# Performance work log

Measured on AMD Instinct MI355X. Metric: run time of the kernel, lower is better.

The kernel has to match this reference:

```python
import jax, jax.numpy as jnp
import numpy as np

H = 4096          # hidden_size
NQ = 32           # num query heads
NKV = 8           # num kv heads
D = 128           # head_dim
GRP = NQ // NKV   # query heads per kv head
THETA = 10000.0
SCALE = D ** -0.5


def _rope(x, positions):
    # x: [S, N, D]; neox-style rotate-half over full head_dim
    half = D // 2
    inv_freq = 1.0 / (THETA ** (jnp.arange(0, half, dtype=jnp.float32) / half * 2.0 * 0.5 * 2))
    inv_freq = 1.0 / (THETA ** (jnp.arange(0, D, 2, dtype=jnp.float32) / D))
    freqs = positions.astype(jnp.float32)[:, None] * inv_freq[None, :]  # [S, D/2]
    cos = jnp.cos(freqs)[:, None, :]  # [S,1,D/2]
    sin = jnp.sin(freqs)[:, None, :]
    x1, x2 = x[..., :half], x[..., half:]
    return jnp.concatenate([x1 * cos - x2 * sin, x2 * cos + x1 * sin], axis=-1)


def setup_inputs() -> dict:
    key = jax.random.key(0)
    k1, k2, k3 = jax.random.split(key, 3)
    S = 4096
    return {
        "positions": jnp.arange(S, dtype=jnp.int64 if jax.config.jax_enable_x64 else jnp.int32),
        "hidden_states": jax.random.normal(k1, (S, H), dtype=jnp.float32) * 0.02,
        "w_qkv": jax.random.normal(k2, (H, NQ * D + 2 * NKV * D), dtype=jnp.float32) * 0.02,
        "w_o": jax.random.normal(k3, (NQ * D, H), dtype=jnp.float32) * 0.02,
    }


def reference(positions, hidden_states, w_qkv, w_o):
    S = hidden_states.shape[0]
    qkv = hidden_states @ w_qkv                         # [S, 6144]
    q, k, v = jnp.split(qkv, [NQ * D, NQ * D + NKV * D], axis=-1)
    q = _rope(q.reshape(S, NQ, D), positions)           # [S, NQ, D]
    k = _rope(k.reshape(S, NKV, D), positions)          # [S, NKV, D]
    v = v.reshape(S, NKV, D)
    # GQA: group query heads per kv head
    qg = q.reshape(S, NKV, GRP, D)
    scores = jnp.einsum('sghd,tgd->ghst', qg, k) * SCALE  # [NKV, GRP, S, S]
    causal = positions[:, None] >= positions[None, :]     # [S, S]
    scores = jnp.where(causal[None, None], scores, jnp.finfo(scores.dtype).min)
    probs = jax.nn.softmax(scores, axis=-1)
    attn = jnp.einsum('ghst,tgd->sghd', probs, v).reshape(S, NQ * D)
    return attn @ w_o
```

## Files before the change

kernel.cpp:

```cpp
#include <hip/hip_runtime.h>
#include <hip/hip_bf16.h>
#include <math.h>

#define H_DIM 4096
#define NQ    32
#define NKV   8
#define HD    128
#define GRPQ  4
#define NQKV  6144
#define KOFF  4096
#define VOFF  5120
#define SCALE 0.08838834764831844f

typedef float f32x4 __attribute__((ext_vector_type(4)));
typedef short bf16x8 __attribute__((ext_vector_type(8)));

static __device__ __forceinline__ float bf2f(unsigned short u) {
    return __uint_as_float(((unsigned int)u) << 16);
}
static __device__ __forceinline__ unsigned short f2bf(float f) {
    return __bfloat16_as_ushort(__float2bfloat16(f));
}

static __device__ __forceinline__ void gload_lds16(const void* g, void* l) {
    __builtin_amdgcn_global_load_lds(
        (const __attribute__((address_space(1))) unsigned int*)g,
        (__attribute__((address_space(3))) unsigned int*)l, 16, 0, 0);
}

static __device__ __forceinline__ float4 load4(const float* p) {
    return *reinterpret_cast<const float4*>(p);
}
static __device__ __forceinline__ float4 load4(const unsigned short* p) {
    ushort4 v = *reinterpret_cast<const ushort4*>(p);
    return make_float4(bf2f(v.x), bf2f(v.y), bf2f(v.z), bf2f(v.w));
}

static __device__ __forceinline__ void store1(float* p, float v) { *p = v; }
static __device__ __forceinline__ void store1(unsigned short* p, float v) {
    *p = f2bf(v);
}

#define BM 128
#define BN 128
#define BK 16
#define LPAD 4

template <typename TA, typename TB, typename TC>
__global__ __launch_bounds__(256) void gemm_f32acc(
    const TA* __restrict__ A,
    const TB* __restrict__ B,
    TC* __restrict__ C,
    int M, int N, int K)
{
    __shared__ float As[BK][BM + LPAD];
    __shared__ float Bs[BK][BN + LPAD];

    const int tid = threadIdx.x;
    const int bm  = blockIdx.y * BM;
    const int bn  = blockIdx.x * BN;
    const int tx  = tid & 15;
    const int ty  = tid >> 4;

    float acc[8][8];
#pragma unroll
    for (int i = 0; i < 8; ++i)
#pragma unroll
        for (int j = 0; j < 8; ++j) acc[i][j] = 0.0f;

    for (int k0 = 0; k0 < K; k0 += BK) {
        for (int q = tid; q < (BM * BK) / 4; q += 256) {
            int row = q >> 2;
            int kq  = (q & 3) << 2;
            float4 v = load4(&A[(size_t)(bm + row) * K + k0 + kq]);
            As[kq + 0][row] = v.x;
            As[kq + 1][row] = v.y;
            As[kq + 2][row] = v.z;
            As[kq + 3][row] = v.w;
        }
        for (int q = tid; q < (BK * BN) / 4; q += 256) {
            int k = q >> 5;
            int n = (q & 31) << 2;
            float4 v = load4(&B[(size_t)(k0 + k) * N + bn + n]);
            Bs[k][n + 0] = v.x;
            Bs[k][n + 1] = v.y;
            Bs[k][n + 2] = v.z;
            Bs[k][n + 3] = v.w;
        }
        __syncthreads();

#pragma unroll
        for (int k = 0; k < BK; ++k) {
            float a[8], b[8];
#pragma unroll
            for (int i = 0; i < 8; ++i) a[i] = As[k][ty * 8 + i];
#pragma unroll
            for (int j = 0; j < 8; ++j) b[j] = Bs[k][tx * 8 + j];
#pragma unroll
            for (int i = 0; i < 8; ++i)
#pragma unroll
                for (int j = 0; j < 8; ++j) acc[i][j] += a[i] * b[j];
        }
        __syncthreads();
    }

#pragma unroll
    for (int i = 0; i < 8; ++i) {
        size_t r = (size_t)(bm + ty * 8 + i);
#pragma unroll
        for (int j = 0; j < 8; ++j) {
            int c = bn + tx * 8 + j;
            store1(&C[r * N + c], acc[i][j]);
        }
    }
}

__global__ __launch_bounds__(256) void cvt_f32_bf16(
    const float4* __restrict__ src, ushort4* __restrict__ dst, int n4)
{
    int i = blockIdx.x * 256 + threadIdx.x;
    int stride = gridDim.x * 256;
    for (; i < n4; i += stride) {
        float4 v = src[i];
        dst[i] = make_ushort4(f2bf(v.x), f2bf(v.y), f2bf(v.z), f2bf(v.w));
    }
}

__global__ __launch_bounds__(256) void transpose_f32_bf16(
    const float* __restrict__ src, unsigned short* __restrict__ dst,
    int R, int C)
{
    __shared__ unsigned short tile[32][33];
    const int r0 = blockIdx.y * 32;
    const int c0 = blockIdx.x * 32;
    const int t  = threadIdx.x;
    const int lr  = t >> 3;
    const int lc4 = (t & 7) << 2;

    float4 v = load4(&src[(size_t)(r0 + lr) * C + c0 + lc4]);
    tile[lr][lc4 + 0] = f2bf(v.x);
    tile[lr][lc4 + 1] = f2bf(v.y);
    tile[lr][lc4 + 2] = f2bf(v.z);
    tile[lr][lc4 + 3] = f2bf(v.w);
    __syncthreads();

    ushort4 o = make_ushort4(tile[lc4 + 0][lr], tile[lc4 + 1][lr],
                             tile[lc4 + 2][lr], tile[lc4 + 3][lr]);
    *reinterpret_cast<ushort4*>(&dst[(size_t)(c0 + lr) * R + r0 + lc4]) = o;
}

template <typename TC>
__global__ __launch_bounds__(256) void gemm_bf16_bt(
    const unsigned short* __restrict__ A,
    const unsigned short* __restrict__ BT,
    TC* __restrict__ C,
    int M, int N, int K)
{
    __shared__ unsigned short As[128 * 32];
    __shared__ unsigned short Bs[128 * 32];

    const int tid  = threadIdx.x;
    const int lane = tid & 63;
    const int w    = tid >> 6;
    const int wr   = w >> 1;
    const int wc   = w & 1;
    const int l15  = lane & 15;
    const int l4   = lane >> 4;
    const size_t bm = (size_t)blockIdx.y * 128;
    const size_t bn = (size_t)blockIdx.x * 128;

    f32x4 acc[4][4];
#pragma unroll
    for (int mi = 0; mi < 4; ++mi)
#pragma unroll
        for (int ni = 0; ni < 4; ++ni) acc[mi][ni] = (f32x4){0.f, 0.f, 0.f, 0.f};

    for (int k0 = 0; k0 < K; k0 += 32) {
        __syncthreads();
#pragma unroll
        for (int it = 0; it < 2; ++it) {
            const int cb = (w * 2 + it) * 64;
            const int c  = cb + lane;
            gload_lds16(A  + (bm + (c >> 2)) * K + k0 + (c & 3) * 8,
                        (char*)As + cb * 16);
            gload_lds16(BT + (bn + (c >> 2)) * K + k0 + (c & 3) * 8,
                        (char*)Bs + cb * 16);
        }
        __syncthreads();

        bf16x8 a[4], b[4];
#pragma unroll
        for (int mi = 0; mi < 4; ++mi)
            a[mi] = *reinterpret_cast<const bf16x8*>(
                (char*)As + (wr * 64 + mi * 16 + l15) * 64 + l4 * 16);
#pragma unroll
        for (int ni = 0; ni < 4; ++ni)
            b[ni] = *reinterpret_cast<const bf16x8*>(
                (char*)Bs + (wc * 64 + ni * 16 + l15) * 64 + l4 * 16);
#pragma unroll
        for (int mi = 0; mi < 4; ++mi)
#pragma unroll
            for (int ni = 0; ni < 4; ++ni)
                acc[mi][ni] = __builtin_amdgcn_mfma_f32_16x16x32_bf16(
                    a[mi], b[ni], acc[mi][ni], 0, 0, 0);
    }

#pragma unroll
    for (int mi = 0; mi < 4; ++mi) {
#pragma unroll
        for (int r = 0; r < 4; ++r) {
            size_t row = bm + wr * 64 + mi * 16 + l4 * 4 + r;
#pragma unroll
            for (int ni = 0; ni < 4; ++ni) {
                size_t col = bn + wc * 64 + ni * 16 + l15;
                store1(&C[row * N + col], acc[mi][ni][r]);
            }
        }
    }
}

__global__ __launch_bounds__(256) void rope_kernel(
    unsigned short* __restrict__ qkv,
    const int* __restrict__ pos32,
    int S)
{
    int idx = blockIdx.x * 256 + threadIdx.x;
    int total = S * (NQ + NKV) * (HD / 2);
    if (idx >= total) return;

    int j    = idx & 63;
    int head = (idx >> 6) % (NQ + NKV);
    int s    = idx / (64 * (NQ + NKV));

    const bool is64 = (pos32[1] == 0);
    int pos = is64 ? pos32[2 * s] : pos32[s];

    unsigned short* row = qkv + (size_t)s * NQKV + head * HD;
    float x1 = bf2f(row[j]);
    float x2 = bf2f(row[j + 64]);

    float p = (float)pos;
    float inv_freq = powf(10000.0f, -((float)j) * (1.0f / 64.0f));
    float f = p * inv_freq;
    float sn, cs;
    sincosf(f, &sn, &cs);

    row[j]      = f2bf(x1 * cs - x2 * sn);
    row[j + 64] = f2bf(x2 * cs + x1 * sn);
}

__global__ __launch_bounds__(256) void attn_mfma(
    const unsigned short* __restrict__ qkv,
    unsigned short* __restrict__ attn_out,
    int S)
{
    __shared__ unsigned short Ks[64 * 128];
    __shared__ unsigned short Vts[128 * 64];
    __shared__ float Ss[4][16 * 68];

    const int tid  = threadIdx.x;
    const int lane = tid & 63;
    const int w    = tid >> 6;
    const int l15  = lane & 15;
    const int l4   = lane >> 4;
    const int h    = blockIdx.y;
    const int g    = h >> 2;
    const int s0   = blockIdx.x * 64;

    bf16x8 qf[4];
    {
        const unsigned short* qrow =
            qkv + (size_t)(s0 + w * 16 + l15) * NQKV + h * HD;
#pragma unroll
        for (int ks = 0; ks < 4; ++ks)
            qf[ks] = *reinterpret_cast<const bf16x8*>(qrow + ks * 32 + l4 * 8);
    }

    f32x4 oacc[8];
#pragma unroll
    for (int dt = 0; dt < 8; ++dt) oacc[dt] = (f32x4){0.f, 0.f, 0.f, 0.f};
    float m_r = -1e30f;
    float l_r = 0.0f;

    const int nt = blockIdx.x + 1;
    for (int t = 0; t < nt; ++t) {
        const int t0 = t * 64;
        __syncthreads();

#pragma unroll
        for (int it = 0; it < 4; ++it) {
            int cc  = tid + it * 256;
            int key = cc >> 4;
            int c   = cc & 15;
            bf16x8 v = *reinterpret_cast<const bf16x8*>(
                qkv + (size_t)(t0 + key) * NQKV + KOFF + g * HD + c * 8);
            *reinterpret_cast<bf16x8*>(
                reinterpret_cast<char*>(Ks) + key * 256 + ((c ^ (key & 7)) << 4)) = v;
        }
#pragma unroll
        for (int it = 0; it < 4; ++it) {
            int cc  = tid + it * 256;
            int key = cc & 63;
            int d0  = (cc >> 6) * 8;
            bf16x8 v = *reinterpret_cast<const bf16x8*>(
                qkv + (size_t)(t0 + key) * NQKV + VOFF + g * HD + d0);
#pragma unroll
            for (int j = 0; j < 8; ++j) {
                *reinterpret_cast<unsigned short*>(
                    reinterpret_cast<char*>(Vts) + (d0 + j) * 128 +
                    (((key >> 3) ^ j) << 4) + (key & 7) * 2) = (unsigned short)v[j];
            }
        }
        __syncthreads();

        f32x4 sacc[4];
#pragma unroll
        for (int ct = 0; ct < 4; ++ct) sacc[ct] = (f32x4){0.f, 0.f, 0.f, 0.f};
#pragma unroll
        for (int ct = 0; ct < 4; ++ct) {
            const int key = ct * 16 + l15;
            const char* krow = reinterpret_cast<const char*>(Ks) + key * 256;
            const int swz = (key & 7);
#pragma unroll
            for (int ks = 0; ks < 4; ++ks) {
                int cK = ks * 4 + l4;
                bf16x8 kb = *reinterpret_cast<const bf16x8*>(
                    krow + ((cK ^ swz) << 4));
                sacc[ct] = __builtin_amdgcn_mfma_f32_16x16x32_bf16(
                    qf[ks], kb, sacc[ct], 0, 0, 0);
            }
        }

        const bool diag = (t == nt - 1);
        float* ss = Ss[w];
#pragma unroll
        for (int ct = 0; ct < 4; ++ct) {
            const int key = ct * 16 + l15;
#pragma unroll
            for (int r = 0; r < 4; ++r) {
                int qrow = l4 * 4 + r;
                float v = sacc[ct][r] * SCALE;
                if (diag && key > w * 16 + qrow) v = -1e30f;
                ss[qrow * 68 + key] = v;
            }
        }

        float p[16];
        float mloc = -1e30f;
        const float* srow = ss + l15 * 68;
#pragma unroll
        for (int x = 0; x < 16; ++x) {
            int key = (x >> 3) * 32 + l4 * 8 + (x & 7);
            p[x] = srow[key];
            mloc = fmaxf(mloc, p[x]);
        }
        mloc = fmaxf(mloc, __shfl_xor(mloc, 16));
        mloc = fmaxf(mloc, __shfl_xor(mloc, 32));
        float mnew  = fmaxf(m_r, mloc);
        float alpha = __expf(m_r - mnew);
        float lsum  = 0.f;
#pragma unroll
        for (int x = 0; x < 16; ++x) {
            p[x] = __expf(p[x] - mnew);
            lsum += p[x];
        }
        lsum += __shfl_xor(lsum, 16);
        lsum += __shfl_xor(lsum, 32);
        l_r = l_r * alpha + lsum;
        m_r = mnew;

        bf16x8 pa[2];
#pragma unroll
        for (int ks2 = 0; ks2 < 2; ++ks2)
#pragma unroll
            for (int x = 0; x < 8; ++x)
                pa[ks2][x] = (short)f2bf(p[ks2 * 8 + x]);

#pragma unroll
        for (int r = 0; r < 4; ++r) {
            float ar = __shfl(alpha, l4 * 4 + r);
#pragma unroll
            for (int dt = 0; dt < 8; ++dt) oacc[dt][r] *= ar;
        }

#pragma unroll
        for (int dt = 0; dt < 8; ++dt) {
            const int d   = dt * 16 + l15;
            const char* vrow = reinterpret_cast<const char*>(Vts) + d * 128;
            const int swz = (d & 7);
#pragma unroll
            for (int ks2 = 0; ks2 < 2; ++ks2) {
                int cV = ks2 * 4 + l4;
                bf16x8 vb = *reinterpret_cast<const bf16x8*>(
                    vrow + ((cV ^ swz) << 4));
                oacc[dt] = __builtin_amdgcn_mfma_f32_16x16x32_bf16(
                    pa[ks2], vb, oacc[dt], 0, 0, 0);
            }
        }
    }

#pragma unroll
    for (int r = 0; r < 4; ++r) {
        float lr  = __shfl(l_r, l4 * 4 + r);
        float inv = 1.0f / lr;
        unsigned short* dst =
            attn_out + (size_t)(s0 + w * 16 + l4 * 4 + r) * (NQ * HD) + h * HD;
#pragma unroll
        for (int dt = 0; dt < 8; ++dt)
            dst[dt * 16 + l15] = f2bf(oacc[dt][r] * inv);
    }
}

extern "C" void kernel_launch(void* const* d_in, const int* in_sizes, int n_in,
                              void* d_out, int out_size, void* d_ws, size_t ws_size,
                              hipStream_t stream)
{
    const int*   positions = (const int*)d_in[0];
    const float* hidden    = (const float*)d_in[1];
    const float* w_qkv     = (const float*)d_in[2];
    const float* w_o       = (const float*)d_in[3];
    const int S = in_sizes[0];
    const size_t Sz = (size_t)S;

    unsigned short* qkv   = (unsigned short*)d_ws;
    unsigned short* attn  = qkv   + Sz * NQKV;
    unsigned short* hbf   = attn  + Sz * H_DIM;
    unsigned short* wqkvT = hbf   + Sz * H_DIM;
    unsigned short* woT   = wqkvT + (size_t)NQKV * H_DIM;
    const size_t need = (Sz * NQKV + Sz * H_DIM + Sz * H_DIM +
                         (size_t)NQKV * H_DIM + (size_t)H_DIM * H_DIM) *
                        sizeof(unsigned short);

    if (ws_size >= need) {
        int n4 = (S * H_DIM) / 4;
        int cg = (n4 + 255) / 256; if (cg > 2048) cg = 2048;
        cvt_f32_bf16<<<cg, 256, 0, stream>>>(
            (const float4*)hidden, (ushort4*)hbf, n4);
        transpose_f32_bf16<<<dim3(NQKV / 32, H_DIM / 32), 256, 0, stream>>>(
            w_qkv, wqkvT, H_DIM, NQKV);
        transpose_f32_bf16<<<dim3(H_DIM / 32, H_DIM / 32), 256, 0, stream>>>(
            w_o, woT, H_DIM, H_DIM);

        gemm_bf16_bt<unsigned short><<<dim3(NQKV / 128, S / 128), 256, 0, stream>>>(
            hbf, wqkvT, qkv, S, NQKV, H_DIM);

        int total = S * (NQ + NKV) * (HD / 2);
        rope_kernel<<<(total + 255) / 256, 256, 0, stream>>>(qkv, positions, S);

        attn_mfma<<<dim3(S / 64, NQ), 256, 0, stream>>>(qkv, attn, S);

        gemm_bf16_bt<float><<<dim3(H_DIM / 128, S / 128), 256, 0, stream>>>(
            attn, woT, (float*)d_out, S, H_DIM, H_DIM);
    } else {
        gemm_f32acc<float, float, unsigned short>
            <<<dim3(NQKV / BN, S / BM), 256, 0, stream>>>(
                hidden, w_qkv, qkv, S, NQKV, H_DIM);
        int total = S * (NQ + NKV) * (HD / 2);
        rope_kernel<<<(total + 255) / 256, 256, 0, stream>>>(qkv, positions, S);
        attn_mfma<<<dim3(S / 64, NQ), 256, 0, stream>>>(qkv, attn, S);
        gemm_f32acc<unsigned short, float, float>
            <<<dim3(H_DIM / BN, S / BM), 256, 0, stream>>>(
                attn, w_o, (float*)d_out, S, H_DIM, H_DIM);
    }
}
```

Measured before the change: 1.291 ms.

## Restructure flash attention: 128-row query tiles, register softmax, lazy rescale

Each attention block now handles 128 query rows, with each wave owning 32 rows, so every K/V tile loaded into LDS is reused across twice as many queries. The S = K·Qᵀ product keeps scores in registers in the layout the P·V MFMA needs, removing the LDS round-trip for softmax. Other changes: the scale is folded into Q at load time, the online-softmax rescale is skipped unless the running max grows by more than 8, K tiles are loaded with direct global-to-LDS loads, and heavy causal blocks are scheduled first. The costs are higher register pressure (launch bounds now target 2 blocks per CU), waves idling on the last tile, and slightly different rounding from pre-scaling Q in bf16.

Result: faster. 1.071 ms (-17.1%).

```diff
diff --git a/kernel.cpp b/kernel.cpp
--- a/kernel.cpp
+++ b/kernel.cpp
@@ -249,14 +249,13 @@
     row[j + 64] = f2bf(x2 * cs + x1 * sn);
 }
 
-__global__ __launch_bounds__(256) void attn_mfma(
+__global__ __launch_bounds__(256, 2) void attn_mfma(
     const unsigned short* __restrict__ qkv,
     unsigned short* __restrict__ attn_out,
     int S)
 {
     __shared__ unsigned short Ks[64 * 128];
     __shared__ unsigned short Vts[128 * 64];
-    __shared__ float Ss[4][16 * 68];
 
     const int tid  = threadIdx.x;
     const int lane = tid & 63;
@@ -265,149 +264,184 @@
     const int l4   = lane >> 4;
     const int h    = blockIdx.y;
     const int g    = h >> 2;
-    const int s0   = blockIdx.x * 64;
-
-    bf16x8 qf[4];
-    {
+    const int xb   = (int)gridDim.x - 1 - (int)blockIdx.x;
+    const int s0   = xb * 128;
+    const int qw   = s0 + w * 32;
+
+    bf16x8 qf[2][4];
+#pragma unroll
+    for (int qt = 0; qt < 2; ++qt) {
         const unsigned short* qrow =
-            qkv + (size_t)(s0 + w * 16 + l15) * NQKV + h * HD;
-#pragma unroll
-        for (int ks = 0; ks < 4; ++ks)
-            qf[ks] = *reinterpret_cast<const bf16x8*>(qrow + ks * 32 + l4 * 8);
-    }
-
-    f32x4 oacc[8];
-#pragma unroll
-    for (int dt = 0; dt < 8; ++dt) oacc[dt] = (f32x4){0.f, 0.f, 0.f, 0.f};
-    float m_r = -1e30f;
-    float l_r = 0.0f;
-
-    const int nt = blockIdx.x + 1;
-    for (int t = 0; t < nt; ++t) {
+            qkv + (size_t)(qw + qt * 16 + l15) * NQKV + h * HD;
+#pragma unroll
+        for (int ks = 0; ks < 4; ++ks) {
+            bf16x8 v = *reinterpret_cast<const bf16x8*>(qrow + ks * 32 + l4 * 8);
+            bf16x8 o;
+#pragma unroll
+            for (int i = 0; i < 8; ++i)
+                o[i] = (short)f2bf(bf2f((unsigned short)v[i]) * SCALE);
+            qf[qt][ks] = o;
+        }
+    }
+
+    f32x4 oacc[2][8];
+#pragma unroll
+    for (int qt = 0; qt < 2; ++qt)
+#pragma unroll
+        for (int dt = 0; dt < 8; ++dt) oacc[qt][dt] = (f32x4){0.f, 0.f, 0.f, 0.f};
+    float m_r[2] = {-1e30f, -1e30f};
+    float l_r[2] = {0.f, 0.f};
+
+    const int nt_max = 2 * xb + 2;
+    const int nt_w   = 2 * xb + 1 + (w >> 1);
+
+    for (int t = 0; t < nt_max; ++t) {
         const int t0 = t * 64;
         __syncthreads();
 
 #pragma unroll
         for (int it = 0; it < 4; ++it) {
-            int cc  = tid + it * 256;
-            int key = cc >> 4;
-            int c   = cc & 15;
-            bf16x8 v = *reinterpret_cast<const bf16x8*>(
-                qkv + (size_t)(t0 + key) * NQKV + KOFF + g * HD + c * 8);
-            *reinterpret_cast<bf16x8*>(
-                reinterpret_cast<char*>(Ks) + key * 256 + ((c ^ (key & 7)) << 4)) = v;
+            const int seg  = it * 4 + w;
+            const int clin = seg * 64 + lane;
+            const int key  = clin >> 4;
+            const int csrc = (clin & 15) ^ (key & 7);
+            gload_lds16(qkv + (size_t)(t0 + key) * NQKV + KOFF + g * HD + csrc * 8,
+                        (char*)Ks + (size_t)seg * 1024);
         }
 #pragma unroll
         for (int it = 0; it < 4; ++it) {
-            int cc  = tid + it * 256;
-            int key = cc & 63;
-            int d0  = (cc >> 6) * 8;
+            const int cc  = tid + it * 256;
+            const int key = cc & 63;
+            const int d0  = (cc >> 6) * 8;
             bf16x8 v = *reinterpret_cast<const bf16x8*>(
                 qkv + (size_t)(t0 + key) * NQKV + VOFF + g * HD + d0);
+            const int kt   = key >> 4;
+            const int slot = 32 * (kt >> 1) + 8 * ((key >> 2) & 3) +
+                             4 * (kt & 1) + (key & 3);
 #pragma unroll
             for (int j = 0; j < 8; ++j) {
+                const int d = d0 + j;
                 *reinterpret_cast<unsigned short*>(
-                    reinterpret_cast<char*>(Vts) + (d0 + j) * 128 +
-                    (((key >> 3) ^ j) << 4) + (key & 7) * 2) = (unsigned short)v[j];
-            }
-        }
-        __syncthreads();
-
-        f32x4 sacc[4];
-#pragma unroll
-        for (int ct = 0; ct < 4; ++ct) sacc[ct] = (f32x4){0.f, 0.f, 0.f, 0.f};
-#pragma unroll
-        for (int ct = 0; ct < 4; ++ct) {
-            const int key = ct * 16 + l15;
-            const char* krow = reinterpret_cast<const char*>(Ks) + key * 256;
-            const int swz = (key & 7);
+                    (char*)Vts + d * 128 + ((((slot >> 3) ^ (d & 7))) << 4) +
+                    (slot & 7) * 2) = (unsigned short)v[j];
+            }
+        }
+        __syncthreads();
+
+        if (t >= nt_w) continue;
+
+        f32x4 sacc[4][2];
+#pragma unroll
+        for (int kt = 0; kt < 4; ++kt) {
+            sacc[kt][0] = (f32x4){0.f, 0.f, 0.f, 0.f};
+            sacc[kt][1] = (f32x4){0.f, 0.f, 0.f, 0.f};
+        }
+#pragma unroll
+        for (int kt = 0; kt < 4; ++kt) {
+            const int key = kt * 16 + l15;
+            const char* krow = (const char*)Ks + key * 256;
+            const int swz = key & 7;
 #pragma unroll
             for (int ks = 0; ks < 4; ++ks) {
-                int cK = ks * 4 + l4;
                 bf16x8 kb = *reinterpret_cast<const bf16x8*>(
-                    krow + ((cK ^ swz) << 4));
-                sacc[ct] = __builtin_amdgcn_mfma_f32_16x16x32_bf16(
-                    qf[ks], kb, sacc[ct], 0, 0, 0);
-            }
-        }
-
-        const bool diag = (t == nt - 1);
-        float* ss = Ss[w];
-#pragma unroll
-        for (int ct = 0; ct < 4; ++ct) {
-            const int key = ct * 16 + l15;
-#pragma unroll
-            for (int r = 0; r < 4; ++r) {
-                int qrow = l4 * 4 + r;
-                float v = sacc[ct][r] * SCALE;
-                if (diag && key > w * 16 + qrow) v = -1e30f;
-                ss[qrow * 68 + key] = v;
-            }
-        }
-
-        float p[16];
-        float mloc = -1e30f;
-        const float* srow = ss + l15 * 68;
-#pragma unroll
-        for (int x = 0; x < 16; ++x) {
-            int key = (x >> 3) * 32 + l4 * 8 + (x & 7);
-            p[x] = srow[key];
-            mloc = fmaxf(mloc, p[x]);
-        }
-        mloc = fmaxf(mloc, __shfl_xor(mloc, 16));
-        mloc = fmaxf(mloc, __shfl_xor(mloc, 32));
-        float mnew  = fmaxf(m_r, mloc);
-        float alpha = __expf(m_r - mnew);
-        float lsum  = 0.f;
-#pragma unroll
-        for (int x = 0; x < 16; ++x) {
-            p[x] = __expf(p[x] - mnew);
-            lsum += p[x];
-        }
-        lsum += __shfl_xor(lsum, 16);
-        lsum += __shfl_xor(lsum, 32);
-        l_r = l_r * alpha + lsum;
-        m_r = mnew;
-
-        bf16x8 pa[2];
-#pragma unroll
-        for (int ks2 = 0; ks2 < 2; ++ks2)
-#pragma unroll
-            for (int x = 0; x < 8; ++x)
-                pa[ks2][x] = (short)f2bf(p[ks2 * 8 + x]);
-
+                    krow + (((ks * 4 + l4) ^ swz) << 4));
+                sacc[kt][0] = __builtin_amdgcn_mfma_f32_16x16x32_bf16(
+                    kb, qf[0][ks], sacc[kt][0], 0, 0, 0);
+                sacc[kt][1] = __builtin_amdgcn_mfma_f32_16x16x32_bf16(
+                    kb, qf[1][ks], sacc[kt][1], 0, 0, 0);
+            }
+        }
+
+        if (t == nt_w - 1) {
+#pragma unroll
+            for (int kt = 0; kt < 4; ++kt) {
+                const int keyb = t0 + kt * 16 + l4 * 4;
+#pragma unroll
+                for (int qt = 0; qt < 2; ++qt) {
+                    const int qrow = qw + qt * 16 + l15;
+#pragma unroll
+                    for (int r = 0; r < 4; ++r)
+                        if (keyb + r > qrow) sacc[kt][qt][r] = -1e30f;
+                }
+            }
+        }
+
+        float pmax[2];
+#pragma unroll
+        for (int qt = 0; qt < 2; ++qt) {
+            float mx = sacc[0][qt][0];
+#pragma unroll
+            for (int kt = 0; kt < 4; ++kt)
+#pragma unroll
+                for (int r = 0; r < 4; ++r) mx = fmaxf(mx, sacc[kt][qt][r]);
+            mx = fmaxf(mx, __shfl_xor(mx, 16));
+            mx = fmaxf(mx, __shfl_xor(mx, 32));
+            pmax[qt] = mx;
+        }
+        const bool need = (pmax[0] > m_r[0] + 8.f) || (pmax[1] > m_r[1] + 8.f);
+        if (__any(need)) {
+#pragma unroll
+            for (int qt = 0; qt < 2; ++qt) {
+                float mnew  = fmaxf(m_r[qt], pmax[qt]);
+                float alpha = __expf(m_r[qt] - mnew);
+                l_r[qt] *= alpha;
+                m_r[qt]  = mnew;
+#pragma unroll
+                for (int r = 0; r < 4; ++r) {
+                    float ar = __shfl(alpha, l4 * 4 + r);
+#pragma unroll
+                    for (int dt = 0; dt < 8; ++dt) oacc[qt][dt][r] *= ar;
+                }
+            }
+        }
+
+        bf16x8 pa[2][2];
+#pragma unroll
+        for (int qt = 0; qt < 2; ++qt) {
+            float lsum = 0.f;
+#pragma unroll
+            for (int kt = 0; kt < 4; ++kt) {
+#pragma unroll
+                for (int r = 0; r < 4; ++r) {
+                    float p = __expf(sacc[kt][qt][r] - m_r[qt]);
+                    lsum += p;
+                    pa[qt][kt >> 1][4 * (kt & 1) + r] = (short)f2bf(p);
+                }
+            }
+            lsum += __shfl_xor(lsum, 16);
+            lsum += __shfl_xor(lsum, 32);
+            l_r[qt] += lsum;
+        }
+
+#pragma unroll
+        for (int dt = 0; dt < 8; ++dt) {
+            const int d = dt * 16 + l15;
+            const char* vrow = (const char*)Vts + d * 128;
+            const int swz = d & 7;
+#pragma unroll
+            for (int ks2 = 0; ks2 < 2; ++ks2) {
+                bf16x8 vb = *reinterpret_cast<const bf16x8*>(
+                    vrow + (((ks2 * 4 + l4) ^ swz) << 4));
+                oacc[0][dt] = __builtin_amdgcn_mfma_f32_16x16x32_bf16(
+                    pa[0][ks2], vb, oacc[0][dt], 0, 0, 0);
+                oacc[1][dt] = __builtin_amdgcn_mfma_f32_16x16x32_bf16(
+                    pa[1][ks2], vb, oacc[1][dt], 0, 0, 0);
+            }
+        }
+    }
+
+#pragma unroll
+    for (int qt = 0; qt < 2; ++qt) {
+        float linv_own = 1.0f / l_r[qt];
 #pragma unroll
         for (int r = 0; r < 4; ++r) {
-            float ar = __shfl(alpha, l4 * 4 + r);
-#pragma unroll
-            for (int dt = 0; dt < 8; ++dt) oacc[dt][r] *= ar;
-        }
-
-#pragma unroll
-        for (int dt = 0; dt < 8; ++dt) {
-            const int d   = dt * 16 + l15;
-            const char* vrow = reinterpret_cast<const char*>(Vts) + d * 128;
-            const int swz = (d & 7);
-#pragma unroll
-            for (int ks2 = 0; ks2 < 2; ++ks2) {
-                int cV = ks2 * 4 + l4;
-                bf16x8 vb = *reinterpret_cast<const bf16x8*>(
-                    vrow + ((cV ^ swz) << 4));
-                oacc[dt] = __builtin_amdgcn_mfma_f32_16x16x32_bf16(
-                    pa[ks2], vb, oacc[dt], 0, 0, 0);
-            }
-        }
-    }
-
-#pragma unroll
-    for (int r = 0; r < 4; ++r) {
-        float lr  = __shfl(l_r, l4 * 4 + r);
-        float inv = 1.0f / lr;
-        unsigned short* dst =
-            attn_out + (size_t)(s0 + w * 16 + l4 * 4 + r) * (NQ * HD) + h * HD;
-#pragma unroll
-        for (int dt = 0; dt < 8; ++dt)
-            dst[dt * 16 + l15] = f2bf(oacc[dt][r] * inv);
+            float linv = __shfl(linv_own, l4 * 4 + r);
+            const int row = qw + qt * 16 + l4 * 4 + r;
+            unsigned short* dst = attn_out + (size_t)row * (NQ * HD) + h * HD;
+#pragma unroll
+            for (int dt = 0; dt < 8; ++dt)
+                dst[dt * 16 + l15] = f2bf(oacc[qt][dt][r] * linv);
+        }
     }
 }
 
@@ -447,7 +481,7 @@
         int total = S * (NQ + NKV) * (HD / 2);
         rope_kernel<<<(total + 255) / 256, 256, 0, stream>>>(qkv, positions, S);
 
-        attn_mfma<<<dim3(S / 64, NQ), 256, 0, stream>>>(qkv, attn, S);
+        attn_mfma<<<dim3(S / 128, NQ), 256, 0, stream>>>(qkv, attn, S);
 
         gemm_bf16_bt<float><<<dim3(H_DIM / 128, S / 128), 256, 0, stream>>>(
             attn, woT, (float*)d_out, S, H_DIM, H_DIM);
@@ -457,7 +491,7 @@
                 hidden, w_qkv, qkv, S, NQKV, H_DIM);
         int total = S * (NQ + NKV) * (HD / 2);
         rope_kernel<<<(total + 255) / 256, 256, 0, stream>>>(qkv, positions, S);
-        attn_mfma<<<dim3(S / 64, NQ), 256, 0, stream>>>(qkv, attn, S);
+        attn_mfma<<<dim3(S / 128, NQ), 256, 0, stream>>>(qkv, attn, S);
         gemm_f32acc<unsigned short, float, float>
             <<<dim3(H_DIM / BN, S / BM), 256, 0, stream>>>(
                 attn, w_o, (float*)d_out, S, H_DIM, H_DIM);
```
